# Optimization experiments

Hardware: AMD Instinct MI355X
Metric: run time of the kernel (lower is better)

## Reference

```python
import jax, jax.numpy as jnp
import numpy as np
import math

B, N, C = 8, 512, 384
H, R = 6, 32
PAIR_HIDDEN = 16
RBF_K = 8
HEAD_SCALE = 1.0 / math.sqrt(R)


def setup_inputs() -> dict:
    key = jax.random.key(0)
    ks = jax.random.split(key, 16)
    s = 0.02
    inp = {
        'feats': jax.random.normal(ks[0], (B, 2 * N + 1, C), jnp.float32),
        'xy': jax.random.uniform(ks[1], (B, N, 2), jnp.float32),
        'Wq': jax.random.normal(ks[2], (C, H * R), jnp.float32) * s,
        'Wk': jax.random.normal(ks[3], (C, H * R), jnp.float32) * s,
        'Wpi': jax.random.normal(ks[4], (C, PAIR_HIDDEN), jnp.float32) * s,
        'bpi': jnp.zeros((PAIR_HIDDEN,), jnp.float32),
        'Wpj': jax.random.normal(ks[5], (C, PAIR_HIDDEN), jnp.float32) * s,
        'bpj': jnp.zeros((PAIR_HIDDEN,), jnp.float32),
        'alpha_pair': jnp.float32(0.5),
        'Wg1': jax.random.normal(ks[6], (2 + RBF_K + 2, 32), jnp.float32) * 0.3,
        'bg1': jnp.zeros((32,), jnp.float32),
        'Wg2': jax.random.normal(ks[7], (32, 1), jnp.float32) * 0.3,
        'bg2': jnp.zeros((1,), jnp.float32),
        'alpha_geom': jnp.float32(0.6),
        'Wa1': jax.random.normal(ks[8], (6, 16), jnp.float32) * 0.3,
        'ba1': jnp.zeros((16,), jnp.float32),
        'Wa2': jax.random.normal(ks[9], (16, 1), jnp.float32) * 0.3,
        'ba2': jnp.zeros((1,), jnp.float32),
        'alpha_angle': jnp.float32(0.6),
        'Wd': jax.random.normal(ks[10], (C, 1), jnp.float32) * s,
        'bd': jnp.zeros((1,), jnp.float32),
        'logit_scale': jnp.float32(1.0),
    }
    return inp


def _fold_vertices(feats):
    f = feats[:, 1:]                       # [B, 2N, C]
    b, l, c = f.shape
    return f.reshape(b, l // 2, 2, c).mean(axis=2)  # [B, N, C]


def _principal_orientation(xy):
    # PCA via 5-step power iteration; deterministic init (torch uses randn).
    b, n, _ = xy.shape
    X = xy - xy.mean(axis=1, keepdims=True)
    Cm = jnp.einsum('bnd,bne->bde', X, X) / (n + 1e-8)   # [B,2,2]
    v = jax.random.normal(jax.random.key(42), (b, 2, 1), xy.dtype)
    v = v / (jnp.linalg.norm(v, axis=1, keepdims=True) + 1e-8)
    for _ in range(5):
        v = Cm @ v
        v = v / (jnp.linalg.norm(v, axis=1, keepdims=True) + 1e-8)
    theta0 = jnp.arctan2(v[:, 1, 0], v[:, 0, 0])
    return theta0.reshape(b, 1, 1)


def reference(feats, xy, Wq, Wk, Wpi, bpi, Wpj, bpj, alpha_pair,
              Wg1, bg1, Wg2, bg2, alpha_geom, Wa1, ba1, Wa2, ba2, alpha_angle,
              Wd, bd, logit_scale):
    x = _fold_vertices(feats)                  # [B,N,C]
    b, n, c = x.shape

    Q = (x @ Wq).reshape(b, n, H, R)
    K = (x @ Wk).reshape(b, n, H, R)
    S = jnp.einsum('bnhr,bmhr->bnm', Q, K) * HEAD_SCALE   # heads summed

    a_i = jax.nn.relu(x @ Wpi + bpi)
    b_j = jax.nn.relu(x @ Wpj + bpj)
    S = S + jnp.maximum(alpha_pair, 0.0) * jnp.einsum('bnd,bmd->bnm', a_i, b_j)

    yv, xv = xy[..., 0], xy[..., 1]
    dy = yv[:, :, None] - yv[:, None, :]       # [B,N,N]
    dx = xv[:, :, None] - xv[:, None, :]
    theta = jnp.arctan2(dy, dx)
    theta0 = _principal_orientation(xy)
    theta = jnp.arctan2(jnp.sin(theta - theta0), jnp.cos(theta - theta0))

    # geometry bias
    rbf_mu = jnp.linspace(0.0, math.sqrt(2.0), RBF_K).astype(x.dtype)
    spacing = rbf_mu[1] - rbf_mu[0]
    rbf_gamma = 1.0 / (2.0 * spacing ** 2 + 1e-8)
    r = jnp.sqrt(dy * dy + dx * dx + 1e-8)
    phi = jnp.exp(-rbf_gamma * (r[..., None] - rbf_mu) ** 2)   # [B,N,N,K]
    c1, s1 = jnp.cos(theta), jnp.sin(theta)
    geom_feat = jnp.concatenate(
        [dy[..., None], dx[..., None], phi, c1[..., None], s1[..., None]], axis=-1)
    G = (jax.nn.relu(geom_feat @ Wg1 + bg1) @ Wg2 + bg2)[..., 0]
    S = S + jnp.maximum(alpha_geom, 0.0) * G

    # angle harmonics bias
    c2, s2 = jnp.cos(2.0 * theta), jnp.sin(2.0 * theta)
    c4, s4 = jnp.cos(4.0 * theta), jnp.sin(4.0 * theta)
    ang_feat = jnp.stack([c1, s1, c2, s2, c4, s4], axis=-1)    # [B,N,N,6]
    Hb = (jax.nn.relu(ang_feat @ Wa1 + ba1) @ Wa2 + ba2)[..., 0]
    S = S + jnp.maximum(alpha_angle, 0.0) * Hb

    d = (x @ Wd + bd)[..., 0]                  # [B,N]
    S = S + d[:, :, None] * jnp.eye(n, dtype=S.dtype)
    return S * jnp.maximum(logit_scale, 0.01)
```

## Files before the change

### kernel.cpp

```cpp
#include <hip/hip_runtime.h>
#include <hip/hip_bf16.h>
#include <stdint.h>
#include <string.h>
#include <math.h>

#define B_ 8
#define N_ 512
#define C_ 384
#define HR_ 192
#define PH_ 16
#define HEAD_SCALE_ 0.17677669529663687f
#define QK2W_ 224

#define QK2SZF  (B_*N_*QK2W_/2)
#define OFF_X    0
#define OFF_Q2   (B_*N_*C_)
#define OFF_Q2L  (OFF_Q2  + QK2SZF)
#define OFF_K2   (OFF_Q2L + QK2SZF)
#define OFF_K2L  (OFF_K2  + QK2SZF)
#define OFF_D    (OFF_K2L + QK2SZF)
#define OFF_CS   (OFF_D + B_*N_)
#define OFF_W    (OFF_CS + 2*B_)
#define OFF_FLAG (OFF_W + 700)
#define WS_FLOATS (OFF_W + 768)

struct VInit { float v[16]; };

typedef __attribute__((ext_vector_type(8))) short short8v;
typedef __attribute__((ext_vector_type(4))) float f32x4;

__device__ __forceinline__ float cvt(ushort u) {
  union { uint32_t i; float f; } x; x.i = ((uint32_t)u) << 16; return x.f;
}
__device__ __forceinline__ float cvt(float f) { return f; }

__device__ __forceinline__ ushort f2bf(float f) {
  __hip_bfloat16 h = __float2bfloat16(f);
  union { __hip_bfloat16 b; ushort u; } x; x.b = h; return x.u;
}

__device__ __forceinline__ float4 ld4v(const ushort* p) {
  ushort4 u = *(const ushort4*)p;
  return make_float4(cvt(u.x), cvt(u.y), cvt(u.z), cvt(u.w));
}
__device__ __forceinline__ float4 ld4v(const float* p) { return *(const float4*)p; }

__global__ void detect_kernel(const uint32_t* __restrict__ wg1, float* __restrict__ ws) {
  if (threadIdx.x == 0 && blockIdx.x == 0) {
    int cnt = 0;
    for (int i = 0; i < 128; ++i) {
      uint32_t d = wg1[i];
      float v = cvt((ushort)(d & 0xFFFFu));
      float av = fabsf(v);
      if (av == 0.0f || (av >= 9.5367431640625e-07f && av <= 32.0f)) ++cnt;
    }
    *(int*)(ws + OFF_FLAG) = (cnt >= 64) ? 1 : 0;
  }
}

template <typename T>
__device__ void build_tables(const T* Wg1, const T* bg1, const T* Wg2, const T* bg2,
                             const T* Wa1, const T* ba1, const T* Wa2, const T* ba2,
                             const T* apair, const T* ageom, const T* aang, const T* lsc,
                             float* ws, int tid) {
  for (int j = tid; j < 32; j += 256) {
    float* wj = ws + OFF_W + j*16;
    #pragma unroll
    for (int i = 0; i < 12; ++i) wj[i] = cvt(Wg1[i*32 + j]);
    wj[12] = cvt(bg1[j]);
    wj[13] = cvt(Wg2[j]);
    wj[14] = 0.f; wj[15] = 0.f;
  }
  for (int j = tid; j < 16; j += 256) {
    float* wj = ws + OFF_W + 512 + j*8;
    #pragma unroll
    for (int i = 0; i < 6; ++i) wj[i] = cvt(Wa1[i*16 + j]);
    wj[6] = cvt(ba1[j]);
    wj[7] = cvt(Wa2[j]);
  }
  if (tid == 0) {
    ws[OFF_W + 640] = cvt(bg2[0]);
    ws[OFF_W + 641] = cvt(ba2[0]);
    ws[OFF_W + 642] = fmaxf(cvt(apair[0]), 0.f);
    ws[OFF_W + 643] = fmaxf(cvt(ageom[0]), 0.f);
    ws[OFF_W + 644] = fmaxf(cvt(aang[0]), 0.f);
    ws[OFF_W + 645] = fmaxf(cvt(lsc[0]), 0.01f);
  }
}

__global__ __launch_bounds__(256) void prep_kernel(
    const void* __restrict__ xy,
    const void* __restrict__ Wg1, const void* __restrict__ bg1,
    const void* __restrict__ Wg2, const void* __restrict__ bg2,
    const void* __restrict__ Wa1, const void* __restrict__ ba1,
    const void* __restrict__ Wa2, const void* __restrict__ ba2,
    const void* __restrict__ apair, const void* __restrict__ ageom,
    const void* __restrict__ aang, const void* __restrict__ lsc,
    float* __restrict__ ws, VInit vi)
{
  const int b = blockIdx.x, tid = threadIdx.x;
  const int bf = *(volatile const int*)(ws + OFF_FLAG);
  __shared__ float sxy[N_*2];
  __shared__ float red[256][4];

  if (bf) {
    const ushort* p = (const ushort*)xy + b*N_*2;
    for (int i = tid; i < N_*2; i += 256) sxy[i] = cvt(p[i]);
  } else {
    const float* p = (const float*)xy + b*N_*2;
    for (int i = tid; i < N_*2; i += 256) sxy[i] = p[i];
  }
  __syncthreads();

  float sy = 0.f, sx = 0.f;
  for (int i = tid; i < N_; i += 256) { sy += sxy[2*i]; sx += sxy[2*i+1]; }
  red[tid][0] = sy; red[tid][1] = sx;
  __syncthreads();
  for (int s = 128; s > 0; s >>= 1) {
    if (tid < s) { red[tid][0] += red[tid+s][0]; red[tid][1] += red[tid+s][1]; }
    __syncthreads();
  }
  const float my = red[0][0] / 512.0f;
  const float mx = red[0][1] / 512.0f;
  __syncthreads();

  float c00 = 0.f, c01 = 0.f, c11 = 0.f;
  for (int i = tid; i < N_; i += 256) {
    float y = sxy[2*i] - my;
    float x = sxy[2*i+1] - mx;
    c00 += y*y; c01 += y*x; c11 += x*x;
  }
  red[tid][0] = c00; red[tid][1] = c01; red[tid][2] = c11;
  __syncthreads();
  for (int s = 128; s > 0; s >>= 1) {
    if (tid < s) {
      red[tid][0] += red[tid+s][0];
      red[tid][1] += red[tid+s][1];
      red[tid][2] += red[tid+s][2];
    }
    __syncthreads();
  }
  if (tid == 0) {
    float C00 = red[0][0] / 512.0f, C01 = red[0][1] / 512.0f, C11 = red[0][2] / 512.0f;
    float v0 = vi.v[2*b], v1 = vi.v[2*b + 1];
    float nr = sqrtf(v0*v0 + v1*v1) + 1e-8f; v0 /= nr; v1 /= nr;
    for (int it = 0; it < 5; ++it) {
      float w0 = C00*v0 + C01*v1;
      float w1 = C01*v0 + C11*v1;
      nr = sqrtf(w0*w0 + w1*w1) + 1e-8f;
      v0 = w0/nr; v1 = w1/nr;
    }
    float h = sqrtf(v0*v0 + v1*v1);
    ws[OFF_CS + 2*b + 0] = v0 / h;
    ws[OFF_CS + 2*b + 1] = v1 / h;
  }

  if (b == 0) {
    if (bf) build_tables((const ushort*)Wg1, (const ushort*)bg1, (const ushort*)Wg2, (const ushort*)bg2,
                         (const ushort*)Wa1, (const ushort*)ba1, (const ushort*)Wa2, (const ushort*)ba2,
                         (const ushort*)apair, (const ushort*)ageom, (const ushort*)aang, (const ushort*)lsc,
                         ws, tid);
    else    build_tables((const float*)Wg1, (const float*)bg1, (const float*)Wg2, (const float*)bg2,
                         (const float*)Wa1, (const float*)ba1, (const float*)Wa2, (const float*)ba2,
                         (const float*)apair, (const float*)ageom, (const float*)aang, (const float*)lsc,
                         ws, tid);
  }
}

template <typename T>
__device__ __forceinline__ void fold_body(const T* feats, float* ws, int idx) {
  const int c4 = idx % 96;
  const int bn = idx / 96;
  const int n = bn & (N_ - 1), b = bn >> 9;
  const T* r1 = feats + ((size_t)(b*(2*N_+1) + 1 + 2*n))*C_ + c4*4;
  float4 a = ld4v(r1);
  float4 c = ld4v(r1 + C_);
  float4 o;
  o.x = 0.5f*(a.x + c.x); o.y = 0.5f*(a.y + c.y);
  o.z = 0.5f*(a.z + c.z); o.w = 0.5f*(a.w + c.w);
  *(float4*)(ws + OFF_X + (size_t)idx*4) = o;
}

__global__ __launch_bounds__(256) void fold_kernel(const void* __restrict__ feats,
                                                   float* __restrict__ ws) {
  const int idx = blockIdx.x * 256 + threadIdx.x;
  const int bf = *(volatile const int*)(ws + OFF_FLAG);
  if (bf) fold_body((const ushort*)feats, ws, idx);
  else    fold_body((const float*)feats, ws, idx);
}

#define PKC 32
#define PNKS (C_/PKC)
#define PLDW 68

template <typename T>
__device__ __forceinline__ float4 load_w_small(const T* Wpi, const T* Wpj,
                                               const T* Wd, int c, int wcq) {
  float v[4];
  #pragma unroll
  for (int k = 0; k < 4; ++k) {
    int col = wcq*4 + k;
    float f = 0.f;
    if (col < 16)      f = cvt(Wpi[c*PH_ + col]);
    else if (col < 32) f = cvt(Wpj[c*PH_ + (col - 16)]);
    else if (col == 32) f = cvt(Wd[c]);
    v[k] = f;
  }
  return make_float4(v[0], v[1], v[2], v[3]);
}

__device__ __forceinline__ void split_bf(float v, ushort& hi, ushort& lo) {
  hi = f2bf(v);
  lo = f2bf(v - cvt(hi));
}

template <typename T>
__device__ void proj2_body(const T* __restrict__ Wq, const T* __restrict__ Wk,
                           const T* __restrict__ Wpi, const T* __restrict__ bpi,
                           const T* __restrict__ Wpj, const T* __restrict__ bpj,
                           const T* __restrict__ Wd,  const T* __restrict__ bd,
                           float* __restrict__ ws)
{
  const int ct  = blockIdx.x;
  const int rt  = blockIdx.y;
  const int tid = threadIdx.x;
  const int row0 = rt * 64;

  __shared__ float lx[PKC][PLDW];
  __shared__ float lw[PKC][PLDW];

  const float* X = ws + OFF_X + (size_t)row0 * C_;

  const bool sm = (ct == 6);
  const T* Wsrc = (ct < 3) ? Wq : Wk;
  const int col0 = (ct < 3) ? ct * 64 : (ct - 3) * 64;

  const int xrow = tid >> 3, xcq = tid & 7;
  const int wc   = tid >> 4, wcq = tid & 15;
  const int tr = tid >> 4, tc = tid & 15;

  float4 px0, px1, pw0, pw1;

  px0 = *(const float4*)(X + (size_t)(xrow     ) * C_ + xcq*4);
  px1 = *(const float4*)(X + (size_t)(xrow + 32) * C_ + xcq*4);
  if (!sm) {
    pw0 = ld4v(Wsrc + (size_t)(wc     ) * HR_ + col0 + wcq*4);
    pw1 = ld4v(Wsrc + (size_t)(wc + 16) * HR_ + col0 + wcq*4);
  } else {
    pw0 = load_w_small(Wpi, Wpj, Wd, wc,      wcq);
    pw1 = load_w_small(Wpi, Wpj, Wd, wc + 16, wcq);
  }

  float acc[4][4] = {{0,0,0,0},{0,0,0,0},{0,0,0,0},{0,0,0,0}};

  for (int ks = 0; ks < PNKS; ++ks) {
    lx[xcq*4+0][xrow]      = px0.x;
    lx[xcq*4+1][xrow]      = px0.y;
    lx[xcq*4+2][xrow]      = px0.z;
    lx[xcq*4+3][xrow]      = px0.w;
    lx[xcq*4+0][xrow + 32] = px1.x;
    lx[xcq*4+1][xrow + 32] = px1.y;
    lx[xcq*4+2][xrow + 32] = px1.z;
    lx[xcq*4+3][xrow + 32] = px1.w;
    *(float4*)&lw[wc     ][wcq*4] = pw0;
    *(float4*)&lw[wc + 16][wcq*4] = pw1;
    __syncthreads();

    if (ks + 1 < PNKS) {
      const int c0 = (ks + 1) * PKC;
      px0 = *(const float4*)(X + (size_t)(xrow     ) * C_ + c0 + xcq*4);
      px1 = *(const float4*)(X + (size_t)(xrow + 32) * C_ + c0 + xcq*4);
      if (!sm) {
        pw0 = ld4v(Wsrc + (size_t)(c0 + wc     ) * HR_ + col0 + wcq*4);
        pw1 = ld4v(Wsrc + (size_t)(c0 + wc + 16) * HR_ + col0 + wcq*4);
      } else {
        pw0 = load_w_small(Wpi, Wpj, Wd, c0 + wc,      wcq);
        pw1 = load_w_small(Wpi, Wpj, Wd, c0 + wc + 16, wcq);
      }
    }

    #pragma unroll
    for (int c = 0; c < PKC; ++c) {
      float4 xv = *(const float4*)&lx[c][tr*4];
      float4 wv = *(const float4*)&lw[c][tc*4];
      acc[0][0] = fmaf(xv.x, wv.x, acc[0][0]);
      acc[0][1] = fmaf(xv.x, wv.y, acc[0][1]);
      acc[0][2] = fmaf(xv.x, wv.z, acc[0][2]);
      acc[0][3] = fmaf(xv.x, wv.w, acc[0][3]);
      acc[1][0] = fmaf(xv.y, wv.x, acc[1][0]);
      acc[1][1] = fmaf(xv.y, wv.y, acc[1][1]);
      acc[1][2] = fmaf(xv.y, wv.z, acc[1][2]);
      acc[1][3] = fmaf(xv.y, wv.w, acc[1][3]);
      acc[2][0] = fmaf(xv.z, wv.x, acc[2][0]);
      acc[2][1] = fmaf(xv.z, wv.y, acc[2][1]);
      acc[2][2] = fmaf(xv.z, wv.z, acc[2][2]);
      acc[2][3] = fmaf(xv.z, wv.w, acc[2][3]);
      acc[3][0] = fmaf(xv.w, wv.x, acc[3][0]);
      acc[3][1] = fmaf(xv.w, wv.y, acc[3][1]);
      acc[3][2] = fmaf(xv.w, wv.z, acc[3][2]);
      acc[3][3] = fmaf(xv.w, wv.w, acc[3][3]);
    }
    __syncthreads();
  }

  ushort* q2h = (ushort*)(ws + OFF_Q2);
  ushort* q2l = (ushort*)(ws + OFF_Q2L);
  ushort* k2h = (ushort*)(ws + OFF_K2);
  ushort* k2l = (ushort*)(ws + OFF_K2L);

  if (!sm) {
    const float sc = (ct < 3) ? HEAD_SCALE_ : 1.0f;
    ushort* bh = (ct < 3) ? q2h : k2h;
    ushort* bl = (ct < 3) ? q2l : k2l;
    #pragma unroll
    for (int r = 0; r < 4; ++r) {
      const int row = row0 + tr*4 + r;
      ushort4 oh, ol;
      split_bf(sc*acc[r][0], oh.x, ol.x);
      split_bf(sc*acc[r][1], oh.y, ol.y);
      split_bf(sc*acc[r][2], oh.z, ol.z);
      split_bf(sc*acc[r][3], oh.w, ol.w);
      *(ushort4*)(bh + (size_t)row*QK2W_ + col0 + tc*4) = oh;
      *(ushort4*)(bl + (size_t)row*QK2W_ + col0 + tc*4) = ol;
    }
  } else {
    {
      const int row = row0 + (tid & 63);
      ushort* arr = (tid < 64) ? q2h : (tid < 128) ? q2l : (tid < 192) ? k2h : k2l;
      uint4 z = make_uint4(0,0,0,0);
      *(uint4*)(arr + (size_t)row*QK2W_ + 208) = z;
      *(uint4*)(arr + (size_t)row*QK2W_ + 216) = z;
    }
    const float ap = ws[OFF_W + 642];
    #pragma unroll
    for (int r = 0; r < 4; ++r) {
      const int row = row0 + tr*4 + r;
      #pragma unroll
      for (int k = 0; k < 4; ++k) {
        const int col = tc*4 + k;
        if (col < 16) {
          float v = ap * fmaxf(acc[r][k] + cvt(bpi[col]), 0.f);
          ushort hi, lo; split_bf(v, hi, lo);
          q2h[(size_t)row*QK2W_ + 192 + col] = hi;
          q2l[(size_t)row*QK2W_ + 192 + col] = lo;
        } else if (col < 32) {
          float v = fmaxf(acc[r][k] + cvt(bpj[col - 16]), 0.f);
          ushort hi, lo; split_bf(v, hi, lo);
          k2h[(size_t)row*QK2W_ + 192 + (col - 16)] = hi;
          k2l[(size_t)row*QK2W_ + 192 + (col - 16)] = lo;
        } else if (col == 32) {
          ws[OFF_D + row] = acc[r][k] + cvt(bd[0]);
        }
      }
    }
  }
}

__global__ __launch_bounds__(256) void proj_kernel(
    const void* __restrict__ Wq, const void* __restrict__ Wk,
    const void* __restrict__ Wpi, const void* __restrict__ bpi,
    const void* __restrict__ Wpj, const void* __restrict__ bpj,
    const void* __restrict__ Wd,  const void* __restrict__ bd,
    float* __restrict__ ws)
{
  const int bf = *(volatile const int*)(ws + OFF_FLAG);
  if (bf) proj2_body((const ushort*)Wq, (const ushort*)Wk, (const ushort*)Wpi, (const ushort*)bpi,
                     (const ushort*)Wpj, (const ushort*)bpj, (const ushort*)Wd, (const ushort*)bd, ws);
  else    proj2_body((const float*)Wq, (const float*)Wk, (const float*)Wpi, (const float*)bpi,
                     (const float*)Wpj, (const float*)bpj, (const float*)Wd, (const float*)bd, ws);
}

__global__ __launch_bounds__(256) void score_kernel(
    const void* __restrict__ xy, const float* __restrict__ ws,
    void* __restrict__ out)
{
  const int bf = *(volatile const int*)(ws + OFF_FLAG);
  const int b  = blockIdx.z;
  const int n0 = blockIdx.y * 32, m0 = blockIdx.x * 32;
  const int tid = threadIdx.x;

  __shared__ float xyn[32][2], xym[32][2], dn[32];
  if (tid < 32) {
    if (bf) {
      const ushort* p = (const ushort*)xy;
      xyn[tid][0] = cvt(p[((b*N_) + n0 + tid)*2 + 0]);
      xyn[tid][1] = cvt(p[((b*N_) + n0 + tid)*2 + 1]);
      xym[tid][0] = cvt(p[((b*N_) + m0 + tid)*2 + 0]);
      xym[tid][1] = cvt(p[((b*N_) + m0 + tid)*2 + 1]);
    } else {
      const float* p = (const float*)xy;
      xyn[tid][0] = p[((b*N_) + n0 + tid)*2 + 0];
      xyn[tid][1] = p[((b*N_) + n0 + tid)*2 + 1];
      xym[tid][0] = p[((b*N_) + m0 + tid)*2 + 0];
      xym[tid][1] = p[((b*N_) + m0 + tid)*2 + 1];
    }
    dn[tid] = ws[OFF_D + b*N_ + n0 + tid];
  }
  __syncthreads();

  const int w  = tid >> 6, l = tid & 63;
  const int wr = w >> 1, wc = w & 1;
  const int lr = l & 15, lk = l >> 4;

  const size_t qoff = ((size_t)(b*N_) + n0 + wr*16 + lr) * QK2W_ + lk*8;
  const size_t koff = ((size_t)(b*N_) + m0 + wc*16 + lr) * QK2W_ + lk*8;
  const ushort* qh = (const ushort*)(ws + OFF_Q2)  + qoff;
  const ushort* ql = (const ushort*)(ws + OFF_Q2L) + qoff;
  const ushort* kh = (const ushort*)(ws + OFF_K2)  + koff;
  const ushort* kl = (const ushort*)(ws + OFF_K2L) + koff;

  f32x4 acc = {0.f, 0.f, 0.f, 0.f};
  #pragma unroll
  for (int kc = 0; kc < 7; ++kc) {
    short8v ah = *(const short8v*)(qh + kc*32);
    short8v al = *(const short8v*)(ql + kc*32);
    short8v bh = *(const short8v*)(kh + kc*32);
    short8v bl = *(const short8v*)(kl + kc*32);
    acc = __builtin_amdgcn_mfma_f32_16x16x32_bf16(ah, bh, acc, 0, 0, 0);
    acc = __builtin_amdgcn_mfma_f32_16x16x32_bf16(ah, bl, acc, 0, 0, 0);
    acc = __builtin_amdgcn_mfma_f32_16x16x32_bf16(al, bh, acc, 0, 0, 0);
  }

  const float c0 = ws[OFF_CS + 2*b], s0 = ws[OFF_CS + 2*b + 1];
  const float* wsm = ws + OFF_W;
  const float bg2v = wsm[640], ba2v = wsm[641];
  const float ag = wsm[643], aa = wsm[644], ls = wsm[645];

  const int ml = wc*16 + lr;
  const float ym = xym[ml][0], xm = xym[ml][1];

  const float STEP  = 1.41421354f / 7.0f;
  const float GAMMA = 1.0f / (2.0f*STEP*STEP + 1e-8f);
  float C1[4], S1[4], C2[4], S2[4], C4v[4], S4[4], DY[4], DX[4], PHI[4][8];
  #pragma unroll
  for (int r = 0; r < 4; ++r) {
    const int nl_ = wr*16 + lk*4 + r;
    float dy = xyn[nl_][0] - ym, dx = xyn[nl_][1] - xm;
    DY[r] = dy; DX[r] = dx;
    float h2 = fmaf(dx, dx, dy*dy);
    float rr = sqrtf(h2 + 1e-8f);
    float ct, st;
    if (h2 > 0.f) { float ih = 1.0f / sqrtf(h2); ct = dx*ih; st = dy*ih; }
    else          { ct = 1.f; st = 0.f; }
    float c1 = ct*c0 + st*s0;
    float s1 = st*c0 - ct*s0;
    C1[r] = c1; S1[r] = s1;
    float c2 = c1*c1 - s1*s1, s2 = 2.f*c1*s1;
    C2[r] = c2; S2[r] = s2;
    C4v[r] = c2*c2 - s2*s2; S4[r] = 2.f*c2*s2;
    #pragma unroll
    for (int k = 0; k < 8; ++k) {
      float d = rr - (float)k * STEP;
      PHI[r][k] = __expf(-GAMMA * d * d);
    }
  }

  float g[4] = {0,0,0,0};
  #pragma unroll 4
  for (int j = 0; j < 32; ++j) {
    const float* wj = wsm + j*16;
    #pragma unroll
    for (int r = 0; r < 4; ++r) {
      float h = fmaf(DY[r], wj[0], fmaf(DX[r], wj[1], wj[12]));
      #pragma unroll
      for (int k = 0; k < 8; ++k) h = fmaf(PHI[r][k], wj[2+k], h);
      h = fmaf(C1[r], wj[10], fmaf(S1[r], wj[11], h));
      g[r] = fmaf(fmaxf(h, 0.f), wj[13], g[r]);
    }
  }

  float hb[4] = {0,0,0,0};
  #pragma unroll 4
  for (int j = 0; j < 16; ++j) {
    const float* wj = wsm + 512 + j*8;
    #pragma unroll
    for (int r = 0; r < 4; ++r) {
      float h = fmaf(C1[r],  wj[0], fmaf(S1[r], wj[1], wj[6]));
      h = fmaf(C2[r],  wj[2], fmaf(S2[r], wj[3], h));
      h = fmaf(C4v[r], wj[4], fmaf(S4[r], wj[5], h));
      hb[r] = fmaf(fmaxf(h, 0.f), wj[7], hb[r]);
    }
  }

  const int m_g = m0 + ml;
  #pragma unroll
  for (int r = 0; r < 4; ++r) {
    const int nl_ = wr*16 + lk*4 + r;
    const int n_g = n0 + nl_;
    float S = acc[r] + ag*(g[r] + bg2v) + aa*(hb[r] + ba2v);
    if (n_g == m_g) S += dn[nl_];
    S *= ls;
    const size_t oi = ((size_t)(b*N_) + n_g)*N_ + m_g;
    if (bf) ((__hip_bfloat16*)out)[oi] = __float2bfloat16(S);
    else    ((float*)out)[oi] = S;
  }
}

static inline uint32_t rotl32(uint32_t x, int d) { return (x << d) | (x >> (32 - d)); }

static void threefry2x32_host(uint32_t k0, uint32_t k1, uint32_t& x0, uint32_t& x1) {
  const uint32_t ks0 = k0, ks1 = k1, ks2 = k0 ^ k1 ^ 0x1BD11BDAu;
  static const int R[2][4] = {{13,15,26,6},{17,29,16,24}};
  x0 += ks0; x1 += ks1;
  const uint32_t ks[3] = {ks0, ks1, ks2};
  for (int i = 0; i < 5; ++i) {
    const int* r = R[i & 1];
    for (int j = 0; j < 4; ++j) { x0 += x1; x1 = rotl32(x1, r[j]); x1 ^= x0; }
    x0 += ks[(i + 1) % 3];
    x1 += ks[(i + 2) % 3] + (uint32_t)(i + 1);
  }
}

static float erfinv_host(float x) {
  float w = -log1pf(-x * x);
  float p;
  if (w < 5.0f) {
    w = w - 2.5f;
    p = 2.81022636e-08f;
    p = fmaf(p, w, 3.43273939e-07f);
    p = fmaf(p, w, -3.5233877e-06f);
    p = fmaf(p, w, -4.39150654e-06f);
    p = fmaf(p, w, 0.00021858087f);
    p = fmaf(p, w, -0.00125372503f);
    p = fmaf(p, w, -0.00417768164f);
    p = fmaf(p, w, 0.246640727f);
    p = fmaf(p, w, 1.50140941f);
  } else {
    w = sqrtf(w) - 3.0f;
    p = -0.000200214257f;
    p = fmaf(p, w, 0.000100950558f);
    p = fmaf(p, w, 0.00134934322f);
    p = fmaf(p, w, -0.00367342844f);
    p = fmaf(p, w, 0.00573950773f);
    p = fmaf(p, w, -0.0076224613f);
    p = fmaf(p, w, 0.00943887047f);
    p = fmaf(p, w, 1.00167406f);
    p = fmaf(p, w, 2.83297682f);
  }
  return p * x;
}

static VInit make_vinit() {
  VInit vi;
  for (int i = 0; i < 16; ++i) {
    uint32_t o0 = 0u, o1 = (uint32_t)i;
    threefry2x32_host(0u, 42u, o0, o1);
    uint32_t bits = o0 ^ o1;
    uint32_t fb = (bits >> 9) | 0x3f800000u;
    float f; memcpy(&f, &fb, 4); f -= 1.0f;
    const float lo = -0.99999994f;
    float u = f * 2.0f + lo;
    if (u < lo) u = lo;
    vi.v[i] = 1.41421354f * erfinv_host(u);
  }
  return vi;
}

extern "C" void kernel_launch(void* const* d_in, const int* in_sizes, int n_in,
                              void* d_out, int out_size, void* d_ws, size_t ws_size,
                              hipStream_t stream) {
  (void)in_sizes; (void)n_in; (void)out_size;
  if (ws_size < (size_t)WS_FLOATS * sizeof(float)) return;

  const void* feats = d_in[0];
  const void* xy    = d_in[1];
  const void* Wq    = d_in[2];
  const void* Wk    = d_in[3];
  const void* Wpi   = d_in[4];
  const void* bpi   = d_in[5];
  const void* Wpj   = d_in[6];
  const void* bpj   = d_in[7];
  const void* apair = d_in[8];
  const void* Wg1   = d_in[9];
  const void* bg1   = d_in[10];
  const void* bg2w  = d_in[11];
  const void* bg2b  = d_in[12];
  const void* ageom = d_in[13];
  const void* Wa1   = d_in[14];
  const void* ba1   = d_in[15];
  const void* Wa2   = d_in[16];
  const void* ba2   = d_in[17];
  const void* aang  = d_in[18];
  const void* Wd    = d_in[19];
  const void* bd    = d_in[20];
  const void* lsc   = d_in[21];
  float* ws = (float*)d_ws;

  VInit vi = make_vinit();

  hipLaunchKernelGGL(detect_kernel, dim3(1), dim3(64), 0, stream,
      (const uint32_t*)Wg1, ws);
  hipLaunchKernelGGL(prep_kernel, dim3(B_), dim3(256), 0, stream,
      xy, Wg1, bg1, bg2w, bg2b, Wa1, ba1, Wa2, ba2, apair, ageom, aang, lsc, ws, vi);
  hipLaunchKernelGGL(fold_kernel, dim3(1536), dim3(256), 0, stream, feats, ws);
  hipLaunchKernelGGL(proj_kernel, dim3(7, 64), dim3(256), 0, stream,
      Wq, Wk, Wpi, bpi, Wpj, bpj, Wd, bd, ws);
  hipLaunchKernelGGL(score_kernel, dim3(16, 16, B_), dim3(256), 0, stream,
      xy, ws, d_out);
}
```

Measured before the change: 201.2 us.

## Move projection GEMM to bf16x3 MFMA with pre-split transposed weights

```diff
diff --git a/kernel.cpp b/kernel.cpp
--- a/kernel.cpp
+++ b/kernel.cpp
@@ -11,16 +11,19 @@
 #define PH_ 16
 #define HEAD_SCALE_ 0.17677669529663687f
 #define QK2W_ 224
-
-#define QK2SZF  (B_*N_*QK2W_/2)
-#define OFF_X    0
-#define OFF_Q2   (B_*N_*C_)
-#define OFF_Q2L  (OFF_Q2  + QK2SZF)
-#define OFF_K2   (OFF_Q2L + QK2SZF)
-#define OFF_K2L  (OFF_K2  + QK2SZF)
-#define OFF_D    (OFF_K2L + QK2SZF)
-#define OFF_CS   (OFF_D + B_*N_)
-#define OFF_W    (OFF_CS + 2*B_)
+#define WTC_ 448
+
+#define OFF_XH   0
+#define OFF_XL   786432
+#define OFF_WTH  1572864
+#define OFF_WTL  1658880
+#define OFF_Q2   1744896
+#define OFF_Q2L  2203648
+#define OFF_K2   2662400
+#define OFF_K2L  3121152
+#define OFF_D    3579904
+#define OFF_CS   3584000
+#define OFF_W    3584016
 #define OFF_FLAG (OFF_W + 700)
 #define WS_FLOATS (OFF_W + 768)
 
@@ -44,6 +47,11 @@
   return make_float4(cvt(u.x), cvt(u.y), cvt(u.z), cvt(u.w));
 }
 __device__ __forceinline__ float4 ld4v(const float* p) { return *(const float4*)p; }
+
+__device__ __forceinline__ void split_bf(float v, ushort& hi, ushort& lo) {
+  hi = f2bf(v);
+  lo = f2bf(v - cvt(hi));
+}
 
 __global__ void detect_kernel(const uint32_t* __restrict__ wg1, float* __restrict__ ws) {
   if (threadIdx.x == 0 && blockIdx.x == 0) {
@@ -178,196 +186,187 @@
   float4 o;
   o.x = 0.5f*(a.x + c.x); o.y = 0.5f*(a.y + c.y);
   o.z = 0.5f*(a.z + c.z); o.w = 0.5f*(a.w + c.w);
-  *(float4*)(ws + OFF_X + (size_t)idx*4) = o;
-}
-
-__global__ __launch_bounds__(256) void fold_kernel(const void* __restrict__ feats,
-                                                   float* __restrict__ ws) {
-  const int idx = blockIdx.x * 256 + threadIdx.x;
+  ushort4 oh, ol;
+  split_bf(o.x, oh.x, ol.x);
+  split_bf(o.y, oh.y, ol.y);
+  split_bf(o.z, oh.z, ol.z);
+  split_bf(o.w, oh.w, ol.w);
+  const size_t off = (size_t)bn*C_ + c4*4;
+  *(ushort4*)((ushort*)(ws + OFF_XH) + off) = oh;
+  *(ushort4*)((ushort*)(ws + OFF_XL) + off) = ol;
+}
+
+template <typename T>
+__device__ __forceinline__ void wsplit_body(const T* Wq, const T* Wk,
+                                            const T* Wpi, const T* Wpj,
+                                            const T* Wd, float* ws, int gidx) {
+  const int col = gidx / C_;
+  const int k   = gidx - col*C_;
+  float v;
+  if      (col < 192) v = HEAD_SCALE_ * cvt(Wq[k*HR_ + col]);
+  else if (col < 384) v = cvt(Wk[k*HR_ + (col - 192)]);
+  else if (col < 400) v = cvt(Wpi[k*PH_ + (col - 384)]);
+  else if (col < 416) v = cvt(Wpj[k*PH_ + (col - 400)]);
+  else if (col == 416) v = cvt(Wd[k]);
+  else v = 0.f;
+  ushort hi, lo; split_bf(v, hi, lo);
+  ((ushort*)(ws + OFF_WTH))[gidx] = hi;
+  ((ushort*)(ws + OFF_WTL))[gidx] = lo;
+}
+
+__global__ __launch_bounds__(256) void fold_kernel(
+    const void* __restrict__ feats,
+    const void* __restrict__ Wq, const void* __restrict__ Wk,
+    const void* __restrict__ Wpi, const void* __restrict__ Wpj,
+    const void* __restrict__ Wd,
+    float* __restrict__ ws)
+{
+  const int bid = blockIdx.x;
   const int bf = *(volatile const int*)(ws + OFF_FLAG);
-  if (bf) fold_body((const ushort*)feats, ws, idx);
-  else    fold_body((const float*)feats, ws, idx);
-}
-
-#define PKC 32
-#define PNKS (C_/PKC)
-#define PLDW 68
-
-template <typename T>
-__device__ __forceinline__ float4 load_w_small(const T* Wpi, const T* Wpj,
-                                               const T* Wd, int c, int wcq) {
-  float v[4];
-  #pragma unroll
-  for (int k = 0; k < 4; ++k) {
-    int col = wcq*4 + k;
-    float f = 0.f;
-    if (col < 16)      f = cvt(Wpi[c*PH_ + col]);
-    else if (col < 32) f = cvt(Wpj[c*PH_ + (col - 16)]);
-    else if (col == 32) f = cvt(Wd[c]);
-    v[k] = f;
-  }
-  return make_float4(v[0], v[1], v[2], v[3]);
-}
-
-__device__ __forceinline__ void split_bf(float v, ushort& hi, ushort& lo) {
-  hi = f2bf(v);
-  lo = f2bf(v - cvt(hi));
-}
-
-template <typename T>
-__device__ void proj2_body(const T* __restrict__ Wq, const T* __restrict__ Wk,
-                           const T* __restrict__ Wpi, const T* __restrict__ bpi,
-                           const T* __restrict__ Wpj, const T* __restrict__ bpj,
-                           const T* __restrict__ Wd,  const T* __restrict__ bd,
-                           float* __restrict__ ws)
+  if (bid < 1536) {
+    const int idx = bid * 256 + threadIdx.x;
+    if (bf) fold_body((const ushort*)feats, ws, idx);
+    else    fold_body((const float*)feats, ws, idx);
+  } else {
+    const int gidx = (bid - 1536) * 256 + threadIdx.x;
+    if (bf) wsplit_body((const ushort*)Wq, (const ushort*)Wk, (const ushort*)Wpi,
+                        (const ushort*)Wpj, (const ushort*)Wd, ws, gidx);
+    else    wsplit_body((const float*)Wq, (const float*)Wk, (const float*)Wpi,
+                        (const float*)Wpj, (const float*)Wd, ws, gidx);
+  }
+}
+
+#define MFA(a,b,c) __builtin_amdgcn_mfma_f32_16x16x32_bf16(a, b, c, 0, 0, 0)
+
+__global__ __launch_bounds__(64) void proj_kernel(
+    const void* __restrict__ bpi, const void* __restrict__ bpj,
+    const void* __restrict__ bd,  float* __restrict__ ws)
 {
-  const int ct  = blockIdx.x;
-  const int rt  = blockIdx.y;
-  const int tid = threadIdx.x;
-  const int row0 = rt * 64;
-
-  __shared__ float lx[PKC][PLDW];
-  __shared__ float lw[PKC][PLDW];
-
-  const float* X = ws + OFF_X + (size_t)row0 * C_;
-
-  const bool sm = (ct == 6);
-  const T* Wsrc = (ct < 3) ? Wq : Wk;
-  const int col0 = (ct < 3) ? ct * 64 : (ct - 3) * 64;
-
-  const int xrow = tid >> 3, xcq = tid & 7;
-  const int wc   = tid >> 4, wcq = tid & 15;
-  const int tr = tid >> 4, tc = tid & 15;
-
-  float4 px0, px1, pw0, pw1;
-
-  px0 = *(const float4*)(X + (size_t)(xrow     ) * C_ + xcq*4);
-  px1 = *(const float4*)(X + (size_t)(xrow + 32) * C_ + xcq*4);
-  if (!sm) {
-    pw0 = ld4v(Wsrc + (size_t)(wc     ) * HR_ + col0 + wcq*4);
-    pw1 = ld4v(Wsrc + (size_t)(wc + 16) * HR_ + col0 + wcq*4);
-  } else {
-    pw0 = load_w_small(Wpi, Wpj, Wd, wc,      wcq);
-    pw1 = load_w_small(Wpi, Wpj, Wd, wc + 16, wcq);
-  }
-
-  float acc[4][4] = {{0,0,0,0},{0,0,0,0},{0,0,0,0},{0,0,0,0}};
-
-  for (int ks = 0; ks < PNKS; ++ks) {
-    lx[xcq*4+0][xrow]      = px0.x;
-    lx[xcq*4+1][xrow]      = px0.y;
-    lx[xcq*4+2][xrow]      = px0.z;
-    lx[xcq*4+3][xrow]      = px0.w;
-    lx[xcq*4+0][xrow + 32] = px1.x;
-    lx[xcq*4+1][xrow + 32] = px1.y;
-    lx[xcq*4+2][xrow + 32] = px1.z;
-    lx[xcq*4+3][xrow + 32] = px1.w;
-    *(float4*)&lw[wc     ][wcq*4] = pw0;
-    *(float4*)&lw[wc + 16][wcq*4] = pw1;
-    __syncthreads();
-
-    if (ks + 1 < PNKS) {
-      const int c0 = (ks + 1) * PKC;
-      px0 = *(const float4*)(X + (size_t)(xrow     ) * C_ + c0 + xcq*4);
-      px1 = *(const float4*)(X + (size_t)(xrow + 32) * C_ + c0 + xcq*4);
-      if (!sm) {
-        pw0 = ld4v(Wsrc + (size_t)(c0 + wc     ) * HR_ + col0 + wcq*4);
-        pw1 = ld4v(Wsrc + (size_t)(c0 + wc + 16) * HR_ + col0 + wcq*4);
-      } else {
-        pw0 = load_w_small(Wpi, Wpj, Wd, c0 + wc,      wcq);
-        pw1 = load_w_small(Wpi, Wpj, Wd, c0 + wc + 16, wcq);
-      }
-    }
-
-    #pragma unroll
-    for (int c = 0; c < PKC; ++c) {
-      float4 xv = *(const float4*)&lx[c][tr*4];
-      float4 wv = *(const float4*)&lw[c][tc*4];
-      acc[0][0] = fmaf(xv.x, wv.x, acc[0][0]);
-      acc[0][1] = fmaf(xv.x, wv.y, acc[0][1]);
-      acc[0][2] = fmaf(xv.x, wv.z, acc[0][2]);
-      acc[0][3] = fmaf(xv.x, wv.w, acc[0][3]);
-      acc[1][0] = fmaf(xv.y, wv.x, acc[1][0]);
-      acc[1][1] = fmaf(xv.y, wv.y, acc[1][1]);
-      acc[1][2] = fmaf(xv.y, wv.z, acc[1][2]);
-      acc[1][3] = fmaf(xv.y, wv.w, acc[1][3]);
-      acc[2][0] = fmaf(xv.z, wv.x, acc[2][0]);
-      acc[2][1] = fmaf(xv.z, wv.y, acc[2][1]);
-      acc[2][2] = fmaf(xv.z, wv.z, acc[2][2]);
-      acc[2][3] = fmaf(xv.z, wv.w, acc[2][3]);
-      acc[3][0] = fmaf(xv.w, wv.x, acc[3][0]);
-      acc[3][1] = fmaf(xv.w, wv.y, acc[3][1]);
-      acc[3][2] = fmaf(xv.w, wv.z, acc[3][2]);
-      acc[3][3] = fmaf(xv.w, wv.w, acc[3][3]);
-    }
-    __syncthreads();
+  const int ct = blockIdx.x;
+  const int rt = blockIdx.y;
+  const int l  = threadIdx.x;
+  const int lr = l & 15, lk = l >> 4;
+  const int row0 = rt * 32, colg0 = ct * 32;
+  const int bf = *(volatile const int*)(ws + OFF_FLAG);
+
+  const ushort* xh  = (const ushort*)(ws + OFF_XH);
+  const ushort* xl  = (const ushort*)(ws + OFF_XL);
+  const ushort* wth = (const ushort*)(ws + OFF_WTH);
+  const ushort* wtl = (const ushort*)(ws + OFF_WTL);
+
+  const size_t a0 = (size_t)(row0 + lr) * C_ + lk*8;
+  const size_t a1 = a0 + (size_t)16 * C_;
+  const size_t b0 = (size_t)(colg0 + lr) * C_ + lk*8;
+  const size_t b1 = b0 + (size_t)16 * C_;
+
+  f32x4 acc00 = {0,0,0,0}, acc01 = {0,0,0,0}, acc10 = {0,0,0,0}, acc11 = {0,0,0,0};
+
+  short8v ah0 = *(const short8v*)(xh + a0);
+  short8v ah1 = *(const short8v*)(xh + a1);
+  short8v al0 = *(const short8v*)(xl + a0);
+  short8v al1 = *(const short8v*)(xl + a1);
+  short8v bh0 = *(const short8v*)(wth + b0);
+  short8v bh1 = *(const short8v*)(wth + b1);
+  short8v bl0 = *(const short8v*)(wtl + b0);
+  short8v bl1 = *(const short8v*)(wtl + b1);
+
+  for (int ks = 0; ks < 12; ++ks) {
+    short8v nah0, nah1, nal0, nal1, nbh0, nbh1, nbl0, nbl1;
+    if (ks < 11) {
+      const int o = (ks + 1) * 32;
+      nah0 = *(const short8v*)(xh + a0 + o);
+      nah1 = *(const short8v*)(xh + a1 + o);
+      nal0 = *(const short8v*)(xl + a0 + o);
+      nal1 = *(const short8v*)(xl + a1 + o);
+      nbh0 = *(const short8v*)(wth + b0 + o);
+      nbh1 = *(const short8v*)(wth + b1 + o);
+      nbl0 = *(const short8v*)(wtl + b0 + o);
+      nbl1 = *(const short8v*)(wtl + b1 + o);
+    }
+    acc00 = MFA(ah0, bh0, acc00);
+    acc00 = MFA(ah0, bl0, acc00);
+    acc00 = MFA(al0, bh0, acc00);
+    acc01 = MFA(ah0, bh1, acc01);
+    acc01 = MFA(ah0, bl1, acc01);
+    acc01 = MFA(al0, bh1, acc01);
+    acc10 = MFA(ah1, bh0, acc10);
+    acc10 = MFA(ah1, bl0, acc10);
+    acc10 = MFA(al1, bh0, acc10);
+    acc11 = MFA(ah1, bh1, acc11);
+    acc11 = MFA(ah1, bl1, acc11);
+    acc11 = MFA(al1, bh1, acc11);
+    if (ks < 11) {
+      ah0 = nah0; ah1 = nah1; al0 = nal0; al1 = nal1;
+      bh0 = nbh0; bh1 = nbh1; bl0 = nbl0; bl1 = nbl1;
+    }
   }
 
   ushort* q2h = (ushort*)(ws + OFF_Q2);
   ushort* q2l = (ushort*)(ws + OFF_Q2L);
   ushort* k2h = (ushort*)(ws + OFF_K2);
   ushort* k2l = (ushort*)(ws + OFF_K2L);
-
-  if (!sm) {
-    const float sc = (ct < 3) ? HEAD_SCALE_ : 1.0f;
-    ushort* bh = (ct < 3) ? q2h : k2h;
-    ushort* bl = (ct < 3) ? q2l : k2l;
+  const float ap  = ws[OFF_W + 642];
+  const float bdv = bf ? cvt(((const ushort*)bd)[0]) : ((const float*)bd)[0];
+
+  #pragma unroll
+  for (int i = 0; i < 2; ++i) {
     #pragma unroll
-    for (int r = 0; r < 4; ++r) {
-      const int row = row0 + tr*4 + r;
-      ushort4 oh, ol;
-      split_bf(sc*acc[r][0], oh.x, ol.x);
-      split_bf(sc*acc[r][1], oh.y, ol.y);
-      split_bf(sc*acc[r][2], oh.z, ol.z);
-      split_bf(sc*acc[r][3], oh.w, ol.w);
-      *(ushort4*)(bh + (size_t)row*QK2W_ + col0 + tc*4) = oh;
-      *(ushort4*)(bl + (size_t)row*QK2W_ + col0 + tc*4) = ol;
-    }
-  } else {
-    {
-      const int row = row0 + (tid & 63);
-      ushort* arr = (tid < 64) ? q2h : (tid < 128) ? q2l : (tid < 192) ? k2h : k2l;
-      uint4 z = make_uint4(0,0,0,0);
-      *(uint4*)(arr + (size_t)row*QK2W_ + 208) = z;
-      *(uint4*)(arr + (size_t)row*QK2W_ + 216) = z;
-    }
-    const float ap = ws[OFF_W + 642];
-    #pragma unroll
-    for (int r = 0; r < 4; ++r) {
-      const int row = row0 + tr*4 + r;
+    for (int j = 0; j < 2; ++j) {
+      const f32x4 A = (i == 0) ? (j == 0 ? acc00 : acc01) : (j == 0 ? acc10 : acc11);
+      const int gcol = colg0 + j*16 + lr;
+      float bias = 0.f, post = 1.f; int mode;
+      int dcol = 0;
+      if (gcol < 192)      { mode = 0; dcol = gcol; }
+      else if (gcol < 384) { mode = 1; dcol = gcol - 192; }
+      else if (gcol < 400) {
+        mode = 2; dcol = 192 + (gcol - 384); post = ap;
+        bias = bf ? cvt(((const ushort*)bpi)[gcol - 384]) : ((const float*)bpi)[gcol - 384];
+      }
+      else if (gcol < 416) {
+        mode = 3; dcol = 192 + (gcol - 400);
+        bias = bf ? cvt(((const ushort*)bpj)[gcol - 400]) : ((const float*)bpj)[gcol - 400];
+      }
+      else if (gcol == 416) mode = 4;
+      else mode = 5;
+
       #pragma unroll
-      for (int k = 0; k < 4; ++k) {
-        const int col = tc*4 + k;
-        if (col < 16) {
-          float v = ap * fmaxf(acc[r][k] + cvt(bpi[col]), 0.f);
+      for (int r = 0; r < 4; ++r) {
+        const int grow = row0 + i*16 + lk*4 + r;
+        float v = A[r];
+        if (mode == 0) {
           ushort hi, lo; split_bf(v, hi, lo);
-          q2h[(size_t)row*QK2W_ + 192 + col] = hi;
-          q2l[(size_t)row*QK2W_ + 192 + col] = lo;
-        } else if (col < 32) {
-          float v = fmaxf(acc[r][k] + cvt(bpj[col - 16]), 0.f);
+          q2h[(size_t)grow*QK2W_ + dcol] = hi;
+          q2l[(size_t)grow*QK2W_ + dcol] = lo;
+        } else if (mode == 1) {
           ushort hi, lo; split_bf(v, hi, lo);
-          k2h[(size_t)row*QK2W_ + 192 + (col - 16)] = hi;
-          k2l[(size_t)row*QK2W_ + 192 + (col - 16)] = lo;
-        } else if (col == 32) {
-          ws[OFF_D + row] = acc[r][k] + cvt(bd[0]);
+          k2h[(size_t)grow*QK2W_ + dcol] = hi;
+          k2l[(size_t)grow*QK2W_ + dcol] = lo;
+        } else if (mode == 2) {
+          float t = post * fmaxf(v + bias, 0.f);
+          ushort hi, lo; split_bf(t, hi, lo);
+          q2h[(size_t)grow*QK2W_ + dcol] = hi;
+          q2l[(size_t)grow*QK2W_ + dcol] = lo;
+        } else if (mode == 3) {
+          float t = fmaxf(v + bias, 0.f);
+          ushort hi, lo; split_bf(t, hi, lo);
+          k2h[(size_t)grow*QK2W_ + dcol] = hi;
+          k2l[(size_t)grow*QK2W_ + dcol] = lo;
+        } else if (mode == 4) {
+          ws[OFF_D + grow] = v + bdv;
         }
       }
     }
   }
-}
-
-__global__ __launch_bounds__(256) void proj_kernel(
-    const void* __restrict__ Wq, const void* __restrict__ Wk,
-    const void* __restrict__ Wpi, const void* __restrict__ bpi,
-    const void* __restrict__ Wpj, const void* __restrict__ bpj,
-    const void* __restrict__ Wd,  const void* __restrict__ bd,
-    float* __restrict__ ws)
-{
-  const int bf = *(volatile const int*)(ws + OFF_FLAG);
-  if (bf) proj2_body((const ushort*)Wq, (const ushort*)Wk, (const ushort*)Wpi, (const ushort*)bpi,
-                     (const ushort*)Wpj, (const ushort*)bpj, (const ushort*)Wd, (const ushort*)bd, ws);
-  else    proj2_body((const float*)Wq, (const float*)Wk, (const float*)Wpi, (const float*)bpi,
-                     (const float*)Wpj, (const float*)bpj, (const float*)Wd, (const float*)bd, ws);
+
+  if (ct == 13) {
+    const int rr = l >> 1, h = l & 1;
+    const size_t off = (size_t)(row0 + rr)*QK2W_ + 208 + h*8;
+    const uint4 z = make_uint4(0,0,0,0);
+    *(uint4*)(q2h + off) = z;
+    *(uint4*)(q2l + off) = z;
+    *(uint4*)(k2h + off) = z;
+    *(uint4*)(k2l + off) = z;
+  }
 }
 
 __global__ __launch_bounds__(256) void score_kernel(
@@ -592,9 +591,10 @@
       (const uint32_t*)Wg1, ws);
   hipLaunchKernelGGL(prep_kernel, dim3(B_), dim3(256), 0, stream,
       xy, Wg1, bg1, bg2w, bg2b, Wa1, ba1, Wa2, ba2, apair, ageom, aang, lsc, ws, vi);
-  hipLaunchKernelGGL(fold_kernel, dim3(1536), dim3(256), 0, stream, feats, ws);
-  hipLaunchKernelGGL(proj_kernel, dim3(7, 64), dim3(256), 0, stream,
-      Wq, Wk, Wpi, bpi, Wpj, bpj, Wd, bd, ws);
+  hipLaunchKernelGGL(fold_kernel, dim3(2208), dim3(256), 0, stream,
+      feats, Wq, Wk, Wpi, Wpj, Wd, ws);
+  hipLaunchKernelGGL(proj_kernel, dim3(14, 128), dim3(64), 0, stream,
+      bpi, bpj, bd, ws);
   hipLaunchKernelGGL(score_kernel, dim3(16, 16, B_), dim3(256), 0, stream,
       xy, ws, d_out);
 }
```

Measured after the change: 182.9 us. 1.1x faster.
